# Kernel optimization log

Measured on AMD Instinct MI355X. Metric: run time of the kernel, lower is better.

## Reference

```python
import jax, jax.numpy as jnp
import numpy as np

N = 8192
IN_C = 128
OUT_C = 64
ALPHA = 0.5  # LeakyReLU negative slope
NEG_INF = -9e15


def _xavier(key, shape, gain=1.414):
    fan_in, fan_out = shape[0], shape[-1]
    bound = gain * np.sqrt(6.0 / (fan_in + fan_out))
    return jax.random.uniform(key, shape, jnp.float32, -bound, bound)


def setup_inputs() -> dict:
    key = jax.random.key(0)
    k1, k2, k3, k4 = jax.random.split(key, 4)
    h = jax.random.normal(k1, (N, IN_C), jnp.float32)
    adj = jax.random.randint(k2, (N, N), 0, 2, jnp.int32)
    W = _xavier(k3, (IN_C, OUT_C))
    a = _xavier(k4, (2 * OUT_C, 1))
    return {"h": h, "adj": adj, "W": W, "a": a}


def reference(h, adj, W, a):
    # Wh: [N, out]
    Wh = h @ W
    a1 = a[:OUT_C, 0]   # [out]
    a2 = a[OUT_C:, 0]   # [out]
    # additive attention score e[i, j] = leakyrelu((Wh a1)_i + (Wh a2)_j)
    e = jax.nn.leaky_relu(
        (Wh @ a1)[:, None] + (Wh @ a2)[None, :], negative_slope=ALPHA
    )  # [N, N]
    scores = jnp.where(adj > 0, e, NEG_INF)
    attention = jax.nn.softmax(scores, axis=1)  # masked row softmax
    h_prime = attention @ Wh                    # [N, out]
    return jax.nn.leaky_relu(h_prime, negative_slope=ALPHA)  # concat=True path
```

## Files before the change

kernel.cpp:

```cpp
#include <hip/hip_runtime.h>
#include <hip/hip_bf16.h>

#define NN 8192
#define INC 128
#define OUTC 64

typedef __attribute__((ext_vector_type(8))) short bf16x8;
typedef __attribute__((ext_vector_type(4))) float f32x4;
typedef __attribute__((ext_vector_type(4))) int i32x4;

static __device__ __forceinline__ unsigned short f2bf(float x) {
    unsigned int u = __builtin_bit_cast(unsigned int, x);
    u += 0x7fffu + ((u >> 16) & 1u);
    return (unsigned short)(u >> 16);
}
static __device__ __forceinline__ float bf2f(unsigned short b) {
    unsigned int u = ((unsigned int)b) << 16;
    return __builtin_bit_cast(float, u);
}

__global__ __launch_bounds__(256) void ka_pack(const int* __restrict__ adj,
                                               unsigned long long* __restrict__ msk)
{
    const int lane = threadIdx.x & 63;
    const int wid  = (blockIdx.x * 256 + threadIdx.x) >> 6;
    const int l16  = lane & 15;
    const int g16  = lane >> 4;
#pragma unroll 4
    for (int i = 0; i < 32; ++i) {
        const size_t base = ((size_t)wid * 32 + i) * 256;
        i32x4 v = *(const i32x4*)(adj + base + 4 * lane);
        unsigned int nib = (v[0] > 0 ? 1u : 0u) | (v[1] > 0 ? 2u : 0u)
                         | (v[2] > 0 ? 4u : 0u) | (v[3] > 0 ? 8u : 0u);
        unsigned long long m = (unsigned long long)nib << (4 * l16);
        m |= __shfl_xor(m, 1, 64);
        m |= __shfl_xor(m, 2, 64);
        m |= __shfl_xor(m, 4, 64);
        m |= __shfl_xor(m, 8, 64);
        if (l16 == 0) msk[base / 64 + g16] = m;
    }
}

__global__ __launch_bounds__(256) void k1_wh(const float* __restrict__ h,
                                             const float* __restrict__ W,
                                             const float* __restrict__ a,
                                             unsigned short* __restrict__ whbt,
                                             float* __restrict__ f,
                                             float* __restrict__ g)
{
    const int wave = threadIdx.x >> 6;
    const int ch   = threadIdx.x & 63;
    const int row  = blockIdx.x * 4 + wave;
    const f32x4* h4 = (const f32x4*)(h + (size_t)row * INC);
    float acc = 0.f;
#pragma unroll 8
    for (int k4 = 0; k4 < INC / 4; ++k4) {
        f32x4 hv = h4[k4];
        acc += hv[0] * W[(k4 * 4 + 0) * OUTC + ch];
        acc += hv[1] * W[(k4 * 4 + 1) * OUTC + ch];
        acc += hv[2] * W[(k4 * 4 + 2) * OUTC + ch];
        acc += hv[3] * W[(k4 * 4 + 3) * OUTC + ch];
    }
    __shared__ unsigned short tr[64][4];
    tr[ch][wave] = f2bf(acc);

    float v1 = acc * a[ch];
    float v2 = acc * a[64 + ch];
#pragma unroll
    for (int m = 1; m < 64; m <<= 1) {
        v1 += __shfl_xor(v1, m, 64);
        v2 += __shfl_xor(v2, m, 64);
    }
    if (ch == 0) { f[row] = v1; g[row] = v2; }
    __syncthreads();
    if (wave == 0) {
        ushort4 o = *(const ushort4*)&tr[ch][0];
        *(ushort4*)(whbt + (size_t)ch * NN + blockIdx.x * 4) = o;
    }
}

__global__ __launch_bounds__(256) void k2_gmax(const float* __restrict__ g,
                                               float* __restrict__ gmax)
{
    __shared__ float red[256];
    float m = -1e30f;
    for (int i = threadIdx.x; i < NN; i += 256) m = fmaxf(m, g[i]);
    red[threadIdx.x] = m;
    __syncthreads();
    for (int s = 128; s > 0; s >>= 1) {
        if ((int)threadIdx.x < s) red[threadIdx.x] = fmaxf(red[threadIdx.x], red[threadIdx.x + s]);
        __syncthreads();
    }
    if (threadIdx.x == 0) *gmax = red[0];
}

__global__ __launch_bounds__(256) void k3_attn(const unsigned int* __restrict__ msk,
                                               const unsigned short* __restrict__ whbt,
                                               const float* __restrict__ f,
                                               const float* __restrict__ g,
                                               const float* __restrict__ gmaxp,
                                               float* __restrict__ accP,
                                               float* __restrict__ lP,
                                               int colsPerChunk)
{
    const int lane = threadIdx.x & 63;
    const int wave = threadIdx.x >> 6;
    const int lr16 = lane & 15;
    const int kg   = lane >> 4;
    const int rowBase = blockIdx.x * 64 + wave * 16;
    const int r = rowBase + lr16;
    const int chunk = blockIdx.y;
    const int jStart = chunk * colsPerChunk;

    const float L2E = 1.4426950408889634f;
    const float fr = f[r];
    const float gmax = *gmaxp;
    float mm = fr + gmax;
    mm = fmaxf(mm, 0.5f * mm);
    const float mL = mm * L2E;

    f32x4 acc0 = {0.f, 0.f, 0.f, 0.f};
    f32x4 acc1 = {0.f, 0.f, 0.f, 0.f};
    f32x4 acc2 = {0.f, 0.f, 0.f, 0.f};
    f32x4 acc3 = {0.f, 0.f, 0.f, 0.f};
    float ls = 0.f;

    const unsigned int* mrow = msk + (size_t)r * (NN / 32);
    const unsigned short* wb0 = whbt + (size_t)(0 * 16 + lr16) * NN;
    const unsigned short* wb1 = whbt + (size_t)(1 * 16 + lr16) * NN;
    const unsigned short* wb2 = whbt + (size_t)(2 * 16 + lr16) * NN;
    const unsigned short* wb3 = whbt + (size_t)(3 * 16 + lr16) * NN;

#pragma unroll 2
    for (int j0 = jStart; j0 < jStart + colsPerChunk; j0 += 32) {
        const int jl = j0 + kg * 8;
        unsigned int mw = mrow[j0 >> 5];
        unsigned int myb = (mw >> (kg * 8)) & 0xffu;
        f32x4 g0  = *(const f32x4*)(g + jl);
        f32x4 g1  = *(const f32x4*)(g + jl + 4);
        bf16x8 b0 = *(const bf16x8*)(wb0 + jl);
        bf16x8 b1 = *(const bf16x8*)(wb1 + jl);
        bf16x8 b2 = *(const bf16x8*)(wb2 + jl);
        bf16x8 b3 = *(const bf16x8*)(wb3 + jl);

        bf16x8 af;
#pragma unroll
        for (int t = 0; t < 8; ++t) {
            float gj = (t < 4) ? g0[t] : g1[t - 4];
            float s  = fr + gj;
            float lr = fmaxf(s, 0.5f * s);
            float w  = __builtin_amdgcn_exp2f(lr * L2E - mL);
            w = (myb & (1u << t)) ? w : 0.f;
            unsigned short b = f2bf(w);
            af[t] = (short)b;
            ls += bf2f(b);
        }
        acc0 = __builtin_amdgcn_mfma_f32_16x16x32_bf16(af, b0, acc0, 0, 0, 0);
        acc1 = __builtin_amdgcn_mfma_f32_16x16x32_bf16(af, b1, acc1, 0, 0, 0);
        acc2 = __builtin_amdgcn_mfma_f32_16x16x32_bf16(af, b2, acc2, 0, 0, 0);
        acc3 = __builtin_amdgcn_mfma_f32_16x16x32_bf16(af, b3, acc3, 0, 0, 0);
    }

    ls += __shfl_xor(ls, 16, 64);
    ls += __shfl_xor(ls, 32, 64);
    if (lane < 16) lP[(size_t)chunk * NN + rowBase + lane] = ls;

    float* ap = accP + (size_t)chunk * NN * OUTC;
#pragma unroll
    for (int q = 0; q < 4; ++q) {
        const int rm = rowBase + kg * 4 + q;
        ap[(size_t)rm * OUTC +  0 + lr16] = acc0[q];
        ap[(size_t)rm * OUTC + 16 + lr16] = acc1[q];
        ap[(size_t)rm * OUTC + 32 + lr16] = acc2[q];
        ap[(size_t)rm * OUTC + 48 + lr16] = acc3[q];
    }
}

__global__ __launch_bounds__(256) void k4_final(const float* __restrict__ accP,
                                                const float* __restrict__ lP,
                                                float* __restrict__ out, int js)
{
    const int gid = blockIdx.x * 256 + threadIdx.x;
    const int row = gid >> 6;
    const int ch  = gid & 63;
    float av = 0.f, lv = 0.f;
    for (int c = 0; c < js; ++c) {
        av += accP[((size_t)c * NN + row) * OUTC + ch];
        lv += lP[(size_t)c * NN + row];
    }
    if (lv == 0.f) lv = 1.f;
    const float hv = av / lv;
    out[(size_t)row * OUTC + ch] = fmaxf(hv, 0.5f * hv);
}

extern "C" void kernel_launch(void* const* d_in, const int* in_sizes, int n_in,
                              void* d_out, int out_size, void* d_ws, size_t ws_size,
                              hipStream_t stream)
{
    const float* h   = (const float*)d_in[0];
    const int*   adj = (const int*)d_in[1];
    const float* W   = (const float*)d_in[2];
    const float* a   = (const float*)d_in[3];
    float* out = (float*)d_out;

    char* ws = (char*)d_ws;
    unsigned short* whbt = (unsigned short*)ws;
    size_t off = (size_t)OUTC * NN * sizeof(unsigned short);
    float* f = (float*)(ws + off); off += (size_t)NN * 4;
    float* g = (float*)(ws + off); off += (size_t)NN * 4;
    float* gmax = (float*)(ws + off); off += 256;
    unsigned long long* msk = (unsigned long long*)(ws + off);
    off += (size_t)NN * NN / 8;

    const size_t perChunk = (size_t)NN * OUTC * 4 + (size_t)NN * 4;
    int js = 16;
    while (js > 1 && off + (size_t)js * perChunk > ws_size) js >>= 1;
    float* accP = (float*)(ws + off); off += (size_t)js * NN * OUTC * 4;
    float* lP   = (float*)(ws + off);

    ka_pack<<<dim3(2048), 256, 0, stream>>>(adj, msk);
    k1_wh<<<dim3(NN / 4), 256, 0, stream>>>(h, W, a, whbt, f, g);
    k2_gmax<<<1, 256, 0, stream>>>(g, gmax);
    const int colsPerChunk = NN / js;
    k3_attn<<<dim3(NN / 64, js), 256, 0, stream>>>((const unsigned int*)msk, whbt,
                                                   f, g, gmax, accP, lP, colsPerChunk);
    k4_final<<<dim3(NN * OUTC / 256), 256, 0, stream>>>(accP, lP, out, js);
}
```

Measured before the change: 483.5 us.

## Store Wh in MFMA fragment layout, compute row sums via MFMA, simplify exp math

Wh is now written in a fragment-major layout (8 consecutive columns per channel contiguous), so each lane's B-operand load in the attention kernel is one contiguous 16-byte read instead of four strided rows. The softmax denominator is accumulated with an extra MFMA against a ones vector rather than per-lane scalar adds plus shuffles. The LeakyReLU and exp argument is folded into two FMAs and a max. The projection kernel now handles 8 rows per 512-thread block to fill the new layout. The extra MFMA adds matrix-unit work per iteration in exchange for fewer VALU ops.

```diff
diff --git a/kernel.cpp b/kernel.cpp
--- a/kernel.cpp
+++ b/kernel.cpp
@@ -13,10 +13,6 @@
     unsigned int u = __builtin_bit_cast(unsigned int, x);
     u += 0x7fffu + ((u >> 16) & 1u);
     return (unsigned short)(u >> 16);
-}
-static __device__ __forceinline__ float bf2f(unsigned short b) {
-    unsigned int u = ((unsigned int)b) << 16;
-    return __builtin_bit_cast(float, u);
 }
 
 __global__ __launch_bounds__(256) void ka_pack(const int* __restrict__ adj,
@@ -41,16 +37,17 @@
     }
 }
 
-__global__ __launch_bounds__(256) void k1_wh(const float* __restrict__ h,
+__global__ __launch_bounds__(512) void k1_wh(const float* __restrict__ h,
                                              const float* __restrict__ W,
                                              const float* __restrict__ a,
-                                             unsigned short* __restrict__ whbt,
+                                             unsigned short* __restrict__ whF,
                                              float* __restrict__ f,
                                              float* __restrict__ g)
 {
     const int wave = threadIdx.x >> 6;
     const int ch   = threadIdx.x & 63;
-    const int row  = blockIdx.x * 4 + wave;
+    const int seg  = blockIdx.x;
+    const int row  = seg * 8 + wave;
     const f32x4* h4 = (const f32x4*)(h + (size_t)row * INC);
     float acc = 0.f;
 #pragma unroll 8
@@ -61,7 +58,7 @@
         acc += hv[2] * W[(k4 * 4 + 2) * OUTC + ch];
         acc += hv[3] * W[(k4 * 4 + 3) * OUTC + ch];
     }
-    __shared__ unsigned short tr[64][4];
+    __shared__ unsigned short tr[64][8];
     tr[ch][wave] = f2bf(acc);
 
     float v1 = acc * a[ch];
@@ -73,9 +70,9 @@
     }
     if (ch == 0) { f[row] = v1; g[row] = v2; }
     __syncthreads();
-    if (wave == 0) {
-        ushort4 o = *(const ushort4*)&tr[ch][0];
-        *(ushort4*)(whbt + (size_t)ch * NN + blockIdx.x * 4) = o;
+    if (threadIdx.x < 64) {
+        bf16x8 frag = *(const bf16x8*)&tr[threadIdx.x][0];
+        *(bf16x8*)(whF + ((size_t)seg * 64 + threadIdx.x) * 8) = frag;
     }
 }
 
@@ -95,7 +92,7 @@
 }
 
 __global__ __launch_bounds__(256) void k3_attn(const unsigned int* __restrict__ msk,
-                                               const unsigned short* __restrict__ whbt,
+                                               const unsigned short* __restrict__ whF,
                                                const float* __restrict__ f,
                                                const float* __restrict__ g,
                                                const float* __restrict__ gmaxp,
@@ -117,19 +114,20 @@
     const float gmax = *gmaxp;
     float mm = fr + gmax;
     mm = fmaxf(mm, 0.5f * mm);
-    const float mL = mm * L2E;
+    const float mL  = mm * L2E;
+    const float frE = fr * L2E - mL;
+    const float hm  = -0.5f * mL;
 
     f32x4 acc0 = {0.f, 0.f, 0.f, 0.f};
     f32x4 acc1 = {0.f, 0.f, 0.f, 0.f};
     f32x4 acc2 = {0.f, 0.f, 0.f, 0.f};
     f32x4 acc3 = {0.f, 0.f, 0.f, 0.f};
-    float ls = 0.f;
+    f32x4 accl = {0.f, 0.f, 0.f, 0.f};
+    bf16x8 ones;
+#pragma unroll
+    for (int t = 0; t < 8; ++t) ones[t] = (short)0x3F80;
 
     const unsigned int* mrow = msk + (size_t)r * (NN / 32);
-    const unsigned short* wb0 = whbt + (size_t)(0 * 16 + lr16) * NN;
-    const unsigned short* wb1 = whbt + (size_t)(1 * 16 + lr16) * NN;
-    const unsigned short* wb2 = whbt + (size_t)(2 * 16 + lr16) * NN;
-    const unsigned short* wb3 = whbt + (size_t)(3 * 16 + lr16) * NN;
 
 #pragma unroll 2
     for (int j0 = jStart; j0 < jStart + colsPerChunk; j0 += 32) {
@@ -138,32 +136,34 @@
         unsigned int myb = (mw >> (kg * 8)) & 0xffu;
         f32x4 g0  = *(const f32x4*)(g + jl);
         f32x4 g1  = *(const f32x4*)(g + jl + 4);
-        bf16x8 b0 = *(const bf16x8*)(wb0 + jl);
-        bf16x8 b1 = *(const bf16x8*)(wb1 + jl);
-        bf16x8 b2 = *(const bf16x8*)(wb2 + jl);
-        bf16x8 b3 = *(const bf16x8*)(wb3 + jl);
+        const size_t segB = (size_t)((j0 >> 3) + kg) * 64;
+        bf16x8 b0 = *(const bf16x8*)(whF + (segB +  0 + lr16) * 8);
+        bf16x8 b1 = *(const bf16x8*)(whF + (segB + 16 + lr16) * 8);
+        bf16x8 b2 = *(const bf16x8*)(whF + (segB + 32 + lr16) * 8);
+        bf16x8 b3 = *(const bf16x8*)(whF + (segB + 48 + lr16) * 8);
 
         bf16x8 af;
 #pragma unroll
         for (int t = 0; t < 8; ++t) {
             float gj = (t < 4) ? g0[t] : g1[t - 4];
-            float s  = fr + gj;
-            float lr = fmaxf(s, 0.5f * s);
-            float w  = __builtin_amdgcn_exp2f(lr * L2E - mL);
+            float se = __builtin_fmaf(gj, L2E, frE);
+            float u  = __builtin_fmaf(0.5f, se, hm);
+            float w  = __builtin_amdgcn_exp2f(fmaxf(se, u));
             w = (myb & (1u << t)) ? w : 0.f;
-            unsigned short b = f2bf(w);
-            af[t] = (short)b;
-            ls += bf2f(b);
+            af[t] = (short)f2bf(w);
         }
         acc0 = __builtin_amdgcn_mfma_f32_16x16x32_bf16(af, b0, acc0, 0, 0, 0);
         acc1 = __builtin_amdgcn_mfma_f32_16x16x32_bf16(af, b1, acc1, 0, 0, 0);
         acc2 = __builtin_amdgcn_mfma_f32_16x16x32_bf16(af, b2, acc2, 0, 0, 0);
         acc3 = __builtin_amdgcn_mfma_f32_16x16x32_bf16(af, b3, acc3, 0, 0, 0);
-    }
-
-    ls += __shfl_xor(ls, 16, 64);
-    ls += __shfl_xor(ls, 32, 64);
-    if (lane < 16) lP[(size_t)chunk * NN + rowBase + lane] = ls;
+        accl = __builtin_amdgcn_mfma_f32_16x16x32_bf16(af, ones, accl, 0, 0, 0);
+    }
+
+    if (lr16 == 0) {
+#pragma unroll
+        for (int q = 0; q < 4; ++q)
+            lP[(size_t)chunk * NN + rowBase + kg * 4 + q] = accl[q];
+    }
 
     float* ap = accP + (size_t)chunk * NN * OUTC;
 #pragma unroll
@@ -204,7 +204,7 @@
     float* out = (float*)d_out;
 
     char* ws = (char*)d_ws;
-    unsigned short* whbt = (unsigned short*)ws;
+    unsigned short* whF = (unsigned short*)ws;
     size_t off = (size_t)OUTC * NN * sizeof(unsigned short);
     float* f = (float*)(ws + off); off += (size_t)NN * 4;
     float* g = (float*)(ws + off); off += (size_t)NN * 4;
@@ -219,10 +219,10 @@
     float* lP   = (float*)(ws + off);
 
     ka_pack<<<dim3(2048), 256, 0, stream>>>(adj, msk);
-    k1_wh<<<dim3(NN / 4), 256, 0, stream>>>(h, W, a, whbt, f, g);
+    k1_wh<<<dim3(NN / 8), 512, 0, stream>>>(h, W, a, whF, f, g);
     k2_gmax<<<1, 256, 0, stream>>>(g, gmax);
     const int colsPerChunk = NN / js;
-    k3_attn<<<dim3(NN / 64, js), 256, 0, stream>>>((const unsigned int*)msk, whbt,
+    k3_attn<<<dim3(NN / 64, js), 256, 0, stream>>>((const unsigned int*)msk, whF,
                                                    f, g, gmax, accP, lP, colsPerChunk);
     k4_final<<<dim3(NN * OUTC / 256), 256, 0, stream>>>(accP, lP, out, js);
 }
```

After: 441.5 us. 1.1x faster.
